# Kernel optimization log

Hardware: AMD Instinct MI355X
Metric: run time of the kernel (lower is better)

The kernel has to match this reference:

```python
import jax, jax.numpy as jnp
import numpy as np

N_NODES = 50000
N_EDGES = 800000
IN_DIM = 256
OUT_DIM = 64


def setup_inputs() -> dict:
    key = jax.random.key(0)
    k1, k2, k3, k4 = jax.random.split(key, 4)
    feat = jax.random.normal(k1, (N_NODES, IN_DIM), dtype=jnp.float32)
    W1 = jax.random.normal(k2, (IN_DIM, OUT_DIM), dtype=jnp.float32) / np.sqrt(IN_DIM)
    b1 = jnp.zeros((OUT_DIM,), dtype=jnp.float32)
    W2 = jax.random.normal(k3, (OUT_DIM, OUT_DIM), dtype=jnp.float32) / np.sqrt(OUT_DIM)
    b2 = jnp.zeros((OUT_DIM,), dtype=jnp.float32)
    edge_index = jax.random.randint(k4, (2, N_EDGES), 0, N_NODES, dtype=jnp.int64)
    return {"feat": feat, "W1": W1, "b1": b1, "W2": W2, "b2": b2,
            "edge_index": edge_index}


def _gcn_norm(edge_index, num_nodes):
    # PyG GCNConv default: add self-loops, symmetric normalization.
    loops = jnp.arange(num_nodes, dtype=edge_index.dtype)
    src = jnp.concatenate([edge_index[0], loops])  # [E+N]
    dst = jnp.concatenate([edge_index[1], loops])  # [E+N]
    deg = jax.ops.segment_sum(jnp.ones_like(dst, dtype=jnp.float32), dst,
                              num_segments=num_nodes)
    dinv = jnp.where(deg > 0, jax.lax.rsqrt(deg), 0.0)
    norm = dinv[src] * dinv[dst]  # [E+N]
    return src, dst, norm


def _gcn_conv(x, W, b, src, dst, norm, num_nodes):
    h = x @ W                                   # [N, out]
    msg = h[src] * norm[:, None]                # gather + scale, [E+N, out]
    agg = jax.ops.segment_sum(msg, dst, num_segments=num_nodes)
    return agg + b


def reference(feat, W1, b1, W2, b2, edge_index):
    n = feat.shape[0]
    src, dst, norm = _gcn_norm(edge_index, n)
    # Layer 1: GCNConv -> ReLU (dropout is identity in eval mode)
    z = jax.nn.relu(_gcn_conv(feat, W1, b1, src, dst, norm, n))
    # Layer 2
    z = jax.nn.relu(_gcn_conv(z, W2, b2, src, dst, norm, n))
    return z
```

## Files before the change

kernel.cpp:

```cpp
#include <hip/hip_runtime.h>
#include <hip/hip_bf16.h>

#define N_NODES 50000
#define N_EDGES 800000
#define IN_DIM  256
#define OUT_DIM 64
#define CHUNKE  4096
#define NCHK    196
#define NBKT    196
#define STAGE   12288
#define NP      8

using bf16x8 = __attribute__((ext_vector_type(8))) __bf16;
using f32x4  = __attribute__((ext_vector_type(4))) float;
using u32x4  = __attribute__((ext_vector_type(4))) unsigned int;

#define EPACK(s, d)   ((unsigned)((d) >> 8) << 24 | (unsigned)(s) << 8 | ((d) & 255))
#define E_BIN(p)      ((p) >> 24)
#define E_SRC(p)      (((p) >> 8) & 0xFFFFu)
#define E_DLOW(p)     ((p) & 255u)

union BFu { u32x4 u; bf16x8 b; };

__device__ __forceinline__ void split_pack(float x0, float x1,
                                           unsigned& hi, unsigned& lo) {
    unsigned u0 = __float_as_uint(x0), u1 = __float_as_uint(x1);
    hi = (u1 & 0xFFFF0000u) | (u0 >> 16);
    float h0 = __uint_as_float(u0 & 0xFFFF0000u);
    float h1 = __uint_as_float(u1 & 0xFFFF0000u);
    unsigned r0 = __float_as_uint(x0 - h0);
    unsigned r1 = __float_as_uint(x1 - h1);
    lo = (r1 & 0xFFFF0000u) | (r0 >> 16);
}

__device__ __forceinline__ unsigned short bf16_rn(float x) {
    unsigned u = __float_as_uint(x);
    unsigned r = u + 0x7FFFu + ((u >> 16) & 1u);
    return (unsigned short)(r >> 16);
}

__device__ __forceinline__ float bf2f(unsigned short u) {
    return __uint_as_float((unsigned)u << 16);
}

template <int K>
__device__ __forceinline__ void gemm_body(int gbid, const float* __restrict__ X,
                                          const float* __restrict__ W,
                                          unsigned short* __restrict__ H,
                                          char* lds) {
    constexpr int NS = K / 32;
    const int lane = threadIdx.x & 63;
    const int wave = threadIdx.x >> 6;
    const int lm   = lane & 15;
    const int kg   = lane >> 4;

    BFu bhi[NS], blo[NS];
#pragma unroll
    for (int s = 0; s < NS; ++s) {
#pragma unroll
        for (int jp = 0; jp < 4; ++jp) {
            float w0 = W[(size_t)(s * 32 + kg * 8 + 2 * jp)     * 64 + wave * 16 + lm];
            float w1 = W[(size_t)(s * 32 + kg * 8 + 2 * jp + 1) * 64 + wave * 16 + lm];
            unsigned h, l;
            split_pack(w0, w1, h, l);
            bhi[s].u[jp] = h;
            blo[s].u[jp] = l;
        }
    }

    const int srow = threadIdx.x >> 2;
    const int skc  = (threadIdx.x & 3) * 8;
    int gr = gbid * 64 + srow;
    const float* xs = X + (size_t)((gr < N_NODES) ? gr : (N_NODES - 1)) * K;

    f32x4 acc[4] = {};

    float4 c0 = *(const float4*)(xs + skc);
    float4 c1 = *(const float4*)(xs + skc + 4);

#pragma unroll
    for (int s = 0; s < NS; ++s) {
        unsigned short* a_hi = (unsigned short*)(lds + (s & 1) * 8192);
        unsigned short* a_lo = a_hi + 64 * 32;

        BFu h_, l_;
        unsigned h, l;
        split_pack(c0.x, c0.y, h, l); h_.u[0] = h; l_.u[0] = l;
        split_pack(c0.z, c0.w, h, l); h_.u[1] = h; l_.u[1] = l;
        split_pack(c1.x, c1.y, h, l); h_.u[2] = h; l_.u[2] = l;
        split_pack(c1.z, c1.w, h, l); h_.u[3] = h; l_.u[3] = l;
        *(u32x4*)(a_hi + srow * 32 + skc) = h_.u;
        *(u32x4*)(a_lo + srow * 32 + skc) = l_.u;

        if (s + 1 < NS) {
            c0 = *(const float4*)(xs + (s + 1) * 32 + skc);
            c1 = *(const float4*)(xs + (s + 1) * 32 + skc + 4);
        }

        __syncthreads();

#pragma unroll
        for (int m = 0; m < 4; ++m) {
            BFu ah, al;
            ah.u = *(const u32x4*)(a_hi + (m * 16 + lm) * 32 + kg * 8);
            al.u = *(const u32x4*)(a_lo + (m * 16 + lm) * 32 + kg * 8);
            acc[m] = __builtin_amdgcn_mfma_f32_16x16x32_bf16(ah.b, bhi[s].b, acc[m], 0, 0, 0);
            acc[m] = __builtin_amdgcn_mfma_f32_16x16x32_bf16(ah.b, blo[s].b, acc[m], 0, 0, 0);
            acc[m] = __builtin_amdgcn_mfma_f32_16x16x32_bf16(al.b, bhi[s].b, acc[m], 0, 0, 0);
        }
    }

    const int c = wave * 16 + lm;
#pragma unroll
    for (int m = 0; m < 4; ++m) {
#pragma unroll
        for (int t = 0; t < 4; ++t) {
            int r = gbid * 64 + m * 16 + kg * 4 + t;
            if (r < N_NODES) H[(size_t)r * 64 + c] = bf16_rn(acc[m][t]);
        }
    }
}

template <int K>
__global__ __launch_bounds__(256) void fused_hist_gemm1(const void* __restrict__ edges,
                                                        unsigned* __restrict__ epack,
                                                        int* __restrict__ hist,
                                                        const float* __restrict__ X,
                                                        const float* __restrict__ W,
                                                        unsigned short* __restrict__ H) {
    __shared__ char lds[16384];
    if ((int)blockIdx.x < NCHK) {
        int* h  = (int*)lds;
        int* nz = (int*)(lds + 1024);
        if (threadIdx.x == 0) *nz = 0;
        h[threadIdx.x] = 0;
        __syncthreads();
        if (((const unsigned int*)edges)[2 * threadIdx.x + 1] != 0u) *nz = 1;
        __syncthreads();
        const int is64 = (*nz == 0);
        const int base = blockIdx.x * CHUNKE;
        for (int i = threadIdx.x; i < CHUNKE; i += 256) {
            int e = base + i;
            if (e < N_EDGES) {
                int s, d;
                if (is64) {
                    s = (int)((const long long*)edges)[e];
                    d = (int)((const long long*)edges)[(long long)N_EDGES + e];
                } else {
                    s = ((const int*)edges)[e];
                    d = ((const int*)edges)[(long long)N_EDGES + e];
                }
                epack[e] = EPACK(s, d);
                atomicAdd(&h[d >> 8], 1);
            }
        }
        __syncthreads();
        hist[blockIdx.x * 256 + threadIdx.x] = h[threadIdx.x];
    } else {
        gemm_body<K>((int)blockIdx.x - NCHK, X, W, H, lds);
    }
}

__global__ __launch_bounds__(64) void radix_scan(int* __restrict__ hist,
                                                 int* __restrict__ bsum) {
    const int b = blockIdx.x, l = threadIdx.x;
    int carry = 0;
#pragma unroll
    for (int seg = 0; seg < 4; ++seg) {
        int c = seg * 64 + l;
        int v = (c < NCHK) ? hist[c * 256 + b] : 0;
        int incl = v;
        for (int s = 1; s < 64; s <<= 1) {
            int t = __shfl_up(incl, s);
            if (l >= s) incl += t;
        }
        if (c < NCHK) hist[c * 256 + b] = incl - v + carry;
        carry += __shfl(incl, 63);
    }
    if (l == 0) bsum[b] = carry;
}

__global__ __launch_bounds__(256) void radix_scatter(const unsigned* __restrict__ epack,
                                                     const int* __restrict__ hist,
                                                     const int* __restrict__ bsum,
                                                     unsigned* __restrict__ ebuf) {
    __shared__ int lcur[256];
    __shared__ int sm[256];
    __shared__ int sbase[256];
    const int t = threadIdx.x;
    int v = bsum[t];
    sm[t] = v;
    lcur[t] = 0;
    __syncthreads();
    for (int s = 1; s < 256; s <<= 1) {
        int tv = 0;
        if (t >= s) tv = sm[t - s];
        __syncthreads();
        if (t >= s) sm[t] += tv;
        __syncthreads();
    }
    sbase[t] = sm[t] - v;
    __syncthreads();
    const int base = blockIdx.x * CHUNKE;
    for (int i = t; i < CHUNKE; i += 256) {
        int e = base + i;
        if (e < N_EDGES) {
            unsigned p = epack[e];
            int bin = (int)E_BIN(p);
            int loc = atomicAdd(&lcur[bin], 1);
            int pos = sbase[bin] + hist[blockIdx.x * 256 + bin] + loc;
            ebuf[pos] = p;
        }
    }
}

__global__ __launch_bounds__(256) void bucket_finalize(const unsigned* __restrict__ ebuf,
                                                       const int* __restrict__ bsum,
                                                       float* __restrict__ dinv,
                                                       int* __restrict__ off,
                                                       int* __restrict__ csr_src) {
    __shared__ int hist[256];
    __shared__ int sm[256];
    __shared__ int histp[NP * 256];
    __shared__ int curp[NP * 256];
    __shared__ int stage[STAGE];
    __shared__ int beg_s, end_s;
    const int b = blockIdx.x, t = threadIdx.x;

    int v = bsum[t];
    sm[t] = v;
    __syncthreads();
    for (int s = 1; s < 256; s <<= 1) {
        int tv = 0;
        if (t >= s) tv = sm[t - s];
        __syncthreads();
        if (t >= s) sm[t] += tv;
        __syncthreads();
    }
    if (t == b) { beg_s = sm[t] - v; end_s = sm[t]; }
    __syncthreads();
    const int beg = beg_s, end = end_s, size = end - beg;

    hist[t] = 0;
#pragma unroll
    for (int p = 0; p < NP; ++p) histp[p * 256 + t] = 0;
    __syncthreads();
    for (int e = beg + t; e < end; e += 256) {
        unsigned pk = ebuf[e];
        atomicAdd(&hist[E_DLOW(pk)], 1);
        atomicAdd(&histp[(E_SRC(pk) >> 13) * 256 + E_DLOW(pk)], 1);
    }
    __syncthreads();

    v = hist[t];
    sm[t] = v;
    __syncthreads();
    for (int s = 1; s < 256; s <<= 1) {
        int tv = 0;
        if (t >= s) tv = sm[t - s];
        __syncthreads();
        if (t >= s) sm[t] += tv;
        __syncthreads();
    }
    int pre = sm[t] - v;

    int node = b * 256 + t;
    if (node < N_NODES) {
        off[node] = beg + pre;
        dinv[node] = rsqrtf((float)(v + 1));
    }
    if (b == NBKT - 1 && t == 0) off[N_NODES] = end;

    {
        int running = pre;
#pragma unroll
        for (int p = 0; p < NP; ++p) {
            curp[p * 256 + t] = running;
            running += histp[p * 256 + t];
        }
    }
    __syncthreads();

    if (size <= STAGE) {
        for (int e = beg + t; e < end; e += 256) {
            unsigned pk = ebuf[e];
            int q = atomicAdd(&curp[(E_SRC(pk) >> 13) * 256 + E_DLOW(pk)], 1);
            stage[q] = (int)E_SRC(pk);
        }
        __syncthreads();
        for (int i = t; i < size; i += 256) csr_src[beg + i] = stage[i];
    } else {
        for (int e = beg + t; e < end; e += 256) {
            unsigned pk = ebuf[e];
            int q = atomicAdd(&curp[(E_SRC(pk) >> 13) * 256 + E_DLOW(pk)], 1);
            csr_src[beg + q] = (int)E_SRC(pk);
        }
    }
}

template <int K>
__global__ __launch_bounds__(256) void gemm_mfma(const float* __restrict__ X,
                                                 const float* __restrict__ W,
                                                 unsigned short* __restrict__ H) {
    __shared__ char lds[16384];
    gemm_body<K>((int)blockIdx.x, X, W, H, lds);
}

__global__ __launch_bounds__(256) void agg_csr(const unsigned short* __restrict__ H,
                                               const float* __restrict__ dinv,
                                               const float* __restrict__ b,
                                               const int* __restrict__ off,
                                               const int* __restrict__ csr_src,
                                               float* __restrict__ out) {
    int wid  = (blockIdx.x * 256 + threadIdx.x) >> 6;
    int lane = threadIdx.x & 63;
    if (wid >= N_NODES) return;
    float dd = dinv[wid];
    float acc = bf2f(H[(size_t)wid * 64 + lane]) * dd;
    int beg = off[wid], end = off[wid + 1];
    for (int k0 = beg; k0 < end; k0 += 64) {
        int myk = k0 + lane;
        int   s_l  = (myk < end) ? csr_src[myk] : 0;
        float ds_l = (myk < end) ? dinv[s_l] : 0.f;
        int cnt = min(64, end - k0);
        int i = 0;
        for (; i + 8 <= cnt; i += 8) {
            float v[8], nm[8];
#pragma unroll
            for (int jj = 0; jj < 8; ++jj) {
                int s  = __shfl(s_l, i + jj);
                nm[jj] = __shfl(ds_l, i + jj);
                v[jj]  = bf2f(H[(size_t)s * 64 + lane]);
            }
#pragma unroll
            for (int jj = 0; jj < 8; ++jj) acc = fmaf(v[jj], nm[jj], acc);
        }
        for (; i < cnt; ++i) {
            int   s  = __shfl(s_l, i);
            float nm = __shfl(ds_l, i);
            acc = fmaf(bf2f(H[(size_t)s * 64 + lane]), nm, acc);
        }
    }
    out[(size_t)wid * 64 + lane] = fmaxf(fmaf(acc, dd, b[lane]), 0.f);
}

extern "C" void kernel_launch(void* const* d_in, const int* in_sizes, int n_in,
                              void* d_out, int out_size, void* d_ws, size_t ws_size,
                              hipStream_t stream) {
    const float* feat = (const float*)d_in[0];
    const float* W1   = (const float*)d_in[1];
    const float* b1   = (const float*)d_in[2];
    const float* W2   = (const float*)d_in[3];
    const float* b2   = (const float*)d_in[4];
    const void*  edges = d_in[5];
    float* out = (float*)d_out;

    char* ws = (char*)d_ws;
    const size_t SZ_E = (size_t)N_EDGES * 4;
    int*      bsum    = (int*)(ws + 2048);
    int*      hist    = (int*)(ws + 4096);
    float*    dinv    = (float*)(ws + 4096 + 204800);
    int*      off     = (int*)(ws + 4096 + 2 * 204800);
    size_t o = 4096 + 3 * 204800;
    unsigned* epack   = (unsigned*)(ws + o);      o += SZ_E;
    unsigned* ebuf    = (unsigned*)(ws + o);      o += SZ_E;
    int*      csr_src = (int*)(ws + o);           o += SZ_E;
    unsigned short* H = (unsigned short*)(ws + o);

    const int NB_G = (N_NODES + 63) / 64;
    const int NB_W = (N_NODES * 64 + 255) / 256;

    fused_hist_gemm1<IN_DIM><<<NCHK + NB_G, 256, 0, stream>>>(
        edges, epack, hist, feat, W1, H);
    radix_scan<<<256, 64, 0, stream>>>(hist, bsum);
    radix_scatter<<<NCHK, 256, 0, stream>>>(epack, hist, bsum, ebuf);
    bucket_finalize<<<NBKT, 256, 0, stream>>>(ebuf, bsum, dinv, off, csr_src);

    agg_csr<<<NB_W, 256, 0, stream>>>(H, dinv, b1, off, csr_src, out);

    gemm_mfma<OUT_DIM><<<NB_G, 256, 0, stream>>>(out, W2, H);
    agg_csr<<<NB_W, 256, 0, stream>>>(H, dinv, b2, off, csr_src, out);
}
```

Before: 113.2 us.

## Split H into column halves and aggregate each half in a separate pass

The GEMM now writes H in a column-split layout, two planes of 32 columns each. Aggregation runs as two launches per layer, one per half. Each wave handles two edges per step, with each 32-lane half gathering a 64-byte row slice, and the halves are reduced with a shuffle. The aim is to shrink the gathered working set per pass so it fits better in cache and to raise gather parallelism per wave. In exchange it doubles the aggregation launches and the reads of CSR and dinv, and the loop now always does 32 edge slots per 64-edge chunk, relying on zero-padded norms.

After: 194.6 us. +71.9%, slower.

```diff
diff --git a/kernel.cpp b/kernel.cpp
--- a/kernel.cpp
+++ b/kernel.cpp
@@ -110,13 +110,16 @@
         }
     }
 
-    const int c = wave * 16 + lm;
+    const int c    = wave * 16 + lm;
+    const int half = c >> 5;
+    const int c32  = c & 31;
 #pragma unroll
     for (int m = 0; m < 4; ++m) {
 #pragma unroll
         for (int t = 0; t < 4; ++t) {
             int r = gbid * 64 + m * 16 + kg * 4 + t;
-            if (r < N_NODES) H[(size_t)r * 64 + c] = bf16_rn(acc[m][t]);
+            if (r < N_NODES)
+                H[((size_t)half * N_NODES + r) * 32 + c32] = bf16_rn(acc[m][t]);
         }
     }
 }
@@ -306,42 +309,47 @@
     gemm_body<K>((int)blockIdx.x, X, W, H, lds);
 }
 
-__global__ __launch_bounds__(256) void agg_csr(const unsigned short* __restrict__ H,
-                                               const float* __restrict__ dinv,
-                                               const float* __restrict__ b,
-                                               const int* __restrict__ off,
-                                               const int* __restrict__ csr_src,
-                                               float* __restrict__ out) {
+__global__ __launch_bounds__(256) void agg_half(const unsigned short* __restrict__ H_all,
+                                                const float* __restrict__ dinv,
+                                                const float* __restrict__ b,
+                                                const int* __restrict__ off,
+                                                const int* __restrict__ csr_src,
+                                                float* __restrict__ out,
+                                                int half) {
     int wid  = (blockIdx.x * 256 + threadIdx.x) >> 6;
     int lane = threadIdx.x & 63;
     if (wid >= N_NODES) return;
+    const int col = lane & 31;
+    const int eh  = lane >> 5;
+    const unsigned short* Hh = H_all + (size_t)half * N_NODES * 32;
+
     float dd = dinv[wid];
-    float acc = bf2f(H[(size_t)wid * 64 + lane]) * dd;
+    float acc = 0.f;
     int beg = off[wid], end = off[wid + 1];
     for (int k0 = beg; k0 < end; k0 += 64) {
         int myk = k0 + lane;
         int   s_l  = (myk < end) ? csr_src[myk] : 0;
         float ds_l = (myk < end) ? dinv[s_l] : 0.f;
-        int cnt = min(64, end - k0);
-        int i = 0;
-        for (; i + 8 <= cnt; i += 8) {
+#pragma unroll
+        for (int jb = 0; jb < 4; ++jb) {
             float v[8], nm[8];
 #pragma unroll
             for (int jj = 0; jj < 8; ++jj) {
-                int s  = __shfl(s_l, i + jj);
-                nm[jj] = __shfl(ds_l, i + jj);
-                v[jj]  = bf2f(H[(size_t)s * 64 + lane]);
+                int eidx = 2 * (jb * 8 + jj) + eh;
+                int s  = __shfl(s_l, eidx);
+                nm[jj] = __shfl(ds_l, eidx);
+                v[jj]  = bf2f(Hh[(size_t)s * 32 + col]);
             }
 #pragma unroll
             for (int jj = 0; jj < 8; ++jj) acc = fmaf(v[jj], nm[jj], acc);
         }
-        for (; i < cnt; ++i) {
-            int   s  = __shfl(s_l, i);
-            float nm = __shfl(ds_l, i);
-            acc = fmaf(bf2f(H[(size_t)s * 64 + lane]), nm, acc);
-        }
-    }
-    out[(size_t)wid * 64 + lane] = fmaxf(fmaf(acc, dd, b[lane]), 0.f);
+    }
+    float red = acc + __shfl_xor(acc, 32);
+    float sv  = bf2f(Hh[(size_t)wid * 32 + col]);
+    float tot = fmaf(sv, dd, red);
+    if (lane < 32)
+        out[(size_t)wid * 64 + half * 32 + col] =
+            fmaxf(fmaf(tot, dd, b[half * 32 + col]), 0.f);
 }
 
 extern "C" void kernel_launch(void* const* d_in, const int* in_sizes, int n_in,
@@ -376,8 +384,10 @@
     radix_scatter<<<NCHK, 256, 0, stream>>>(epack, hist, bsum, ebuf);
     bucket_finalize<<<NBKT, 256, 0, stream>>>(ebuf, bsum, dinv, off, csr_src);
 
-    agg_csr<<<NB_W, 256, 0, stream>>>(H, dinv, b1, off, csr_src, out);
+    agg_half<<<NB_W, 256, 0, stream>>>(H, dinv, b1, off, csr_src, out, 0);
+    agg_half<<<NB_W, 256, 0, stream>>>(H, dinv, b1, off, csr_src, out, 1);
 
     gemm_mfma<OUT_DIM><<<NB_G, 256, 0, stream>>>(out, W2, H);
-    agg_csr<<<NB_W, 256, 0, stream>>>(H, dinv, b2, off, csr_src, out);
-}
+    agg_half<<<NB_W, 256, 0, stream>>>(H, dinv, b2, off, csr_src, out, 0);
+    agg_half<<<NB_W, 256, 0, stream>>>(H, dinv, b2, off, csr_src, out, 1);
+}
```
